# Kernel optimization log

Hardware: AMD Instinct MI355X
Metric: run time of the kernel (lower is better)

Reference implementation:

```python
import jax, jax.numpy as jnp
import numpy as np

N_HEADS = 16
THETA = 10000.0


def _rope(x, cos, sin):
    # x: [B,H,S,hd]; pairs are interleaved (x[...,2i], x[...,2i+1]) = complex pair
    xe = x[..., 0::2]
    xo = x[..., 1::2]
    re = xe * cos - xo * sin
    im = xe * sin + xo * cos
    return jnp.stack([re, im], axis=-1).reshape(x.shape)


def setup_inputs() -> dict:
    key = jax.random.key(0)
    k1, k2, k3 = jax.random.split(key, 3)
    B, S, D = 2, 2048, 2048
    x = jax.random.normal(k1, (B, S, D), dtype=jnp.float32)
    Wqkv = jax.random.normal(k2, (D, 3 * D), dtype=jnp.float32) * (D ** -0.5)
    Wo = jax.random.normal(k3, (D, D), dtype=jnp.float32) * (D ** -0.5)
    return {"x": x, "Wqkv": Wqkv, "Wo": Wo}


def reference(x, Wqkv, Wo):
    B, S, D = x.shape
    H = N_HEADS
    hd = D // H
    half = hd // 2

    qkv = x @ Wqkv                                   # [B,S,3D]
    q, k, v = jnp.split(qkv, 3, axis=-1)
    # [B,S,D] -> [B,H,S,hd]
    q = q.reshape(B, S, H, hd).transpose(0, 2, 1, 3)
    k = k.reshape(B, S, H, hd).transpose(0, 2, 1, 3)
    v = v.reshape(B, S, H, hd).transpose(0, 2, 1, 3)

    # RoPE frequencies: thetas = theta^(-2i/hd), freqs = pos outer thetas
    i = jnp.arange(half, dtype=jnp.float32)
    inv = THETA ** (-2.0 * i / hd)
    pos = jnp.arange(S, dtype=jnp.float32)
    freqs = pos[:, None] * inv[None, :]              # [S, half]
    cos = jnp.cos(freqs)[None, None]                 # [1,1,S,half]
    sin = jnp.sin(freqs)[None, None]
    q = _rope(q, cos, sin)
    k = _rope(k, cos, sin)

    scale = 1.0 / jnp.sqrt(jnp.float32(hd))
    scores = jnp.einsum("bhqd,bhkd->bhqk", q, k) * scale
    causal = jnp.tril(jnp.ones((S, S), dtype=bool))
    scores = jnp.where(causal[None, None], scores, -jnp.inf)
    attn = jax.nn.softmax(scores, axis=-1)
    y = jnp.einsum("bhqk,bhkd->bhqd", attn, v)       # [B,H,S,hd]
    y = y.transpose(0, 2, 1, 3).reshape(B, S, D)
    return y @ Wo
```

## Files before the change

kernel.cpp:

```cpp
#include <hip/hip_runtime.h>
#include <hip/hip_bf16.h>

typedef __attribute__((ext_vector_type(4))) float f32x4;
typedef __attribute__((ext_vector_type(8))) short s16x8;
typedef unsigned short u16;
typedef unsigned int u32;

#define MFMA16 __builtin_amdgcn_mfma_f32_16x16x32_bf16

#define GLL16(g, l)                                                        \
  __builtin_amdgcn_global_load_lds(                                        \
      (const __attribute__((address_space(1))) void*)(g),                  \
      (__attribute__((address_space(3))) void*)(l), 16, 0, 0)

__device__ __forceinline__ u16 f2b(float f) {
  u32 x = __builtin_bit_cast(u32, f);
  u32 r = (x + 0x7fffu + ((x >> 16) & 1u)) >> 16;
  return (u16)r;
}
__device__ __forceinline__ float b2f(u16 u) {
  u32 x = ((u32)u) << 16;
  return __builtin_bit_cast(float, x);
}

__global__ __launch_bounds__(256) void k_cvt(const float* __restrict__ in, u16* __restrict__ out) {
  size_t i = ((size_t)blockIdx.x * 256 + threadIdx.x) * 4;
  float4 v = *(const float4*)(in + i);
  ushort4 o; o.x = f2b(v.x); o.y = f2b(v.y); o.z = f2b(v.z); o.w = f2b(v.w);
  *(ushort4*)(out + i) = o;
}

__global__ __launch_bounds__(256) void k_tconv(const float* __restrict__ in, u16* __restrict__ out,
                                               int R, int C) {
  __shared__ u16 tile[64][72];
  int c0 = blockIdx.x * 64, r0 = blockIdx.y * 64;
  int t = threadIdx.x;
#pragma unroll
  for (int p = 0; p < 4; ++p) {
    int idx = p * 1024 + t * 4;
    int row = idx >> 6, col = idx & 63;
    float4 v = *(const float4*)&in[(size_t)(r0 + row) * C + c0 + col];
    tile[row][col]     = f2b(v.x);
    tile[row][col + 1] = f2b(v.y);
    tile[row][col + 2] = f2b(v.z);
    tile[row][col + 3] = f2b(v.w);
  }
  __syncthreads();
#pragma unroll
  for (int p = 0; p < 4; ++p) {
    int idx = p * 1024 + t * 4;
    int row = idx >> 6, col = idx & 63;
    ushort4 o;
    o.x = tile[col][row]; o.y = tile[col + 1][row];
    o.z = tile[col + 2][row]; o.w = tile[col + 3][row];
    *(ushort4*)&out[(size_t)(c0 + row) * R + r0 + col] = o;
  }
}

__global__ __launch_bounds__(256) void k_trv(const u16* __restrict__ v, u16* __restrict__ vt) {
  __shared__ u16 tile[64][72];
  int bh = blockIdx.z;
  int s0 = blockIdx.x * 64, d0 = blockIdx.y * 64;
  const u16* src = v + (size_t)bh * 2048 * 128;
  u16* dst = vt + (size_t)bh * 2048 * 128;
  int t = threadIdx.x;
#pragma unroll
  for (int p = 0; p < 4; ++p) {
    int idx = p * 1024 + t * 4;
    int row = idx >> 6, col = idx & 63;
    ushort4 x = *(const ushort4*)&src[(size_t)(s0 + row) * 128 + d0 + col];
    tile[row][col] = x.x; tile[row][col + 1] = x.y;
    tile[row][col + 2] = x.z; tile[row][col + 3] = x.w;
  }
  __syncthreads();
#pragma unroll
  for (int p = 0; p < 4; ++p) {
    int idx = p * 1024 + t * 4;
    int row = idx >> 6, col = idx & 63;
    ushort4 o;
    o.x = tile[col][row]; o.y = tile[col + 1][row];
    o.z = tile[col + 2][row]; o.w = tile[col + 3][row];
    *(ushort4*)&dst[(size_t)(d0 + row) * 2048 + s0 + col] = o;
  }
}

__global__ __launch_bounds__(256) void k_trig(float2* __restrict__ tab) {
  int t = blockIdx.x * 256 + threadIdx.x;
  int s = t >> 6, i = t & 63;
  float inv = expf(-(float)i * (9.210340371976184f / 64.f));
  float a = (float)s * inv;
  float sn, cs;
  sincosf(a, &sn, &cs);
  tab[t] = make_float2(cs, sn);
}

__global__ __launch_bounds__(256) void k_rope(u16* __restrict__ q, u16* __restrict__ k,
                                              const float2* __restrict__ tab) {
  u16* ptr = blockIdx.y ? k : q;
  size_t tid = (size_t)blockIdx.x * 256 + threadIdx.x;
  int g = (int)(tid & 15);
  int s = (int)((tid >> 4) & 2047);
  int bh = (int)(tid >> 15);
  size_t base = ((size_t)bh * 2048 + s) * 128 + (size_t)g * 8;
  uint4 dv = *(const uint4*)(ptr + base);
  u16* pu = (u16*)&dv;
  const float2* tb = &tab[s * 64 + g * 4];
#pragma unroll
  for (int j = 0; j < 4; ++j) {
    float xe = b2f(pu[2 * j]), xo = b2f(pu[2 * j + 1]);
    float c = tb[j].x, sn = tb[j].y;
    pu[2 * j]     = f2b(xe * c - xo * sn);
    pu[2 * j + 1] = f2b(xe * sn + xo * c);
  }
  *(uint4*)(ptr + base) = dv;
}

template <int MODE>
__global__ __launch_bounds__(512) void k_gemm8(const u16* __restrict__ A, const u16* __restrict__ Bt,
                                               u16* __restrict__ qo, u16* __restrict__ ko,
                                               u16* __restrict__ vo, float* __restrict__ C) {
  constexpr int K = 2048;
  constexpr int NT = K / 64;
  __shared__ u16 sA[3][128 * 64];
  __shared__ u16 sB[3][256 * 64];
  int tid = threadIdx.x;
  int lane = tid & 63, w = tid >> 6;
  int wr = w >> 2, wc = w & 3;
  int lr = lane & 15, lg = lane >> 4;

  int n0 = blockIdx.x * 256;
  int m0 = blockIdx.y * 128;

  int srow = tid >> 3;
  int swzcolb = ((tid & 7) << 4) ^ ((srow & 7) << 4);
  const char* gA = (const char*)(A + (size_t)(m0 + srow) * K) + swzcolb;
  const char* gB = (const char*)(Bt + (size_t)(n0 + srow) * K) + swzcolb;

#define STAGE8(buf, k0)                                                      \
  {                                                                          \
    _Pragma("unroll") for (int rb = 0; rb < 4; ++rb)                         \
        GLL16(gB + ((size_t)rb * 64 * K + (k0)) * 2,                         \
              (char*)&sB[buf][0] + rb * 8192 + tid * 16);                    \
    _Pragma("unroll") for (int ra = 0; ra < 2; ++ra)                         \
        GLL16(gA + ((size_t)ra * 64 * K + (k0)) * 2,                         \
              (char*)&sA[buf][0] + ra * 8192 + tid * 16);                    \
  }

  int colb0 = (lg << 4) ^ ((lr & 7) << 4);
  int aRowByte = (wr * 64 + lr) * 128;
  int bRowByte = (wc * 64 + lr) * 128;

  f32x4 acc[4][4] = {};

  STAGE8(0, 0);
  STAGE8(1, 64);

  for (int t = 0; t < NT; ++t) {
    int cur = t % 3;
    const char* sAb = (const char*)&sA[0][0] + cur * (128 * 64 * 2);
    const char* sBb = (const char*)&sB[0][0] + cur * (256 * 64 * 2);
    if (t + 1 < NT) { asm volatile("s_waitcnt vmcnt(6)" ::: "memory"); }
    else            { asm volatile("s_waitcnt vmcnt(0)" ::: "memory"); }
    __builtin_amdgcn_s_barrier();
    if (t + 2 < NT) STAGE8((t + 2) % 3, (t + 2) * 64);
    s16x8 af[4], bf[4];
#pragma unroll
    for (int i = 0; i < 4; ++i) af[i] = *(const s16x8*)(sAb + aRowByte + i * 2048 + colb0);
#pragma unroll
    for (int i = 0; i < 4; ++i) bf[i] = *(const s16x8*)(sBb + bRowByte + i * 2048 + colb0);
    __builtin_amdgcn_s_barrier();
    asm volatile("s_waitcnt lgkmcnt(0)" ::: "memory");
    __builtin_amdgcn_sched_barrier(0);
    __builtin_amdgcn_s_setprio(1);
#pragma unroll
    for (int mi = 0; mi < 4; ++mi)
#pragma unroll
      for (int ni = 0; ni < 4; ++ni)
        acc[mi][ni] = MFMA16(af[mi], bf[ni], acc[mi][ni], 0, 0, 0);
    __builtin_amdgcn_s_setprio(0);
    __builtin_amdgcn_s_barrier();
#pragma unroll
    for (int i = 0; i < 4; ++i) af[i] = *(const s16x8*)(sAb + aRowByte + i * 2048 + (colb0 ^ 64));
#pragma unroll
    for (int i = 0; i < 4; ++i) bf[i] = *(const s16x8*)(sBb + bRowByte + i * 2048 + (colb0 ^ 64));
    __builtin_amdgcn_s_barrier();
    asm volatile("s_waitcnt lgkmcnt(0)" ::: "memory");
    __builtin_amdgcn_sched_barrier(0);
    __builtin_amdgcn_s_setprio(1);
#pragma unroll
    for (int mi = 0; mi < 4; ++mi)
#pragma unroll
      for (int ni = 0; ni < 4; ++ni)
        acc[mi][ni] = MFMA16(af[mi], bf[ni], acc[mi][ni], 0, 0, 0);
    __builtin_amdgcn_s_setprio(0);
  }
#undef STAGE8

  if constexpr (MODE == 0) {
#pragma unroll
    for (int ni = 0; ni < 4; ++ni) {
      int n = n0 + wc * 64 + ni * 16 + lr;
      int which = n >> 11;
      int h = (n >> 7) & 15;
      int d = n & 127;
      u16* dst = which == 0 ? qo : (which == 1 ? ko : vo);
#pragma unroll
      for (int mi = 0; mi < 4; ++mi)
#pragma unroll
        for (int r = 0; r < 4; ++r) {
          int m = m0 + wr * 64 + mi * 16 + lg * 4 + r;
          int b = m >> 11, s = m & 2047;
          dst[(((size_t)b * 16 + h) * 2048 + s) * 128 + d] = f2b(acc[mi][ni][r]);
        }
    }
  } else {
#pragma unroll
    for (int mi = 0; mi < 4; ++mi)
#pragma unroll
      for (int ni = 0; ni < 4; ++ni)
#pragma unroll
        for (int r = 0; r < 4; ++r) {
          int m = m0 + wr * 64 + mi * 16 + lg * 4 + r;
          int n = n0 + wc * 64 + ni * 16 + lr;
          C[(size_t)m * 2048 + n] = acc[mi][ni][r];
        }
  }
}

__global__ __launch_bounds__(256) void k_attn(const u16* __restrict__ q, const u16* __restrict__ k,
                                              const u16* __restrict__ vt, u16* __restrict__ y) {
  constexpr int S = 2048, HD = 128;
  __shared__ u16 kt[2][64][128];
  __shared__ u16 vtl[2][128][64];
  __shared__ u16 pl[4][16][72];
  int bh = blockIdx.x;
  int qt = (gridDim.y - 1) - blockIdx.y;
  int q0 = qt * 64;
  int t = threadIdx.x, lane = t & 63, w = t >> 6;
  int lr = lane & 15, lg = lane >> 4;
  const size_t base = (size_t)bh * S * HD;
  const u16* kbh = k + base;
  const u16* vbh = vt + base;

  int kr_l = ((w * 4) << 2) + (lane >> 4);
  int kcb_base = (lane & 15) << 4;
  int vr_l = ((w * 4) << 3) + (lane >> 3);
  int vcb_base = (lane & 7) << 4;

  s16x8 aq[4];
  {
    size_t qrow = base + (size_t)(q0 + w * 16 + lr) * HD;
#pragma unroll
    for (int i = 0; i < 4; ++i) aq[i] = *(const s16x8*)&q[qrow + i * 32 + lg * 8];
  }
  f32x4 o[8] = {};
  float mrow[4] = {-INFINITY, -INFINITY, -INFINITY, -INFINITY};
  float lsum[4] = {};
  const float scale = 0.08838834764831845f;
  int kv_end = q0 + 64;

#define STAGE_KV(buf, kv)                                                             \
  {                                                                                   \
    _Pragma("unroll")                                                                 \
    for (int i = 0; i < 4; ++i) {                                                     \
      int kr = kr_l + 4 * i;                                                          \
      int kcb = kcb_base ^ ((kr & 7) << 4);                                           \
      GLL16((const char*)(kbh + (size_t)((kv) + kr) * HD) + kcb,                      \
            (char*)&kt[buf][0][0] + ((w * 4 + i) << 10) + (lane << 4));               \
      int vr = vr_l + 8 * i;                                                          \
      int vcb = vcb_base ^ ((vr & 7) << 4);                                           \
      GLL16((const char*)(vbh + (size_t)vr * S + (kv)) + vcb,                         \
            (char*)&vtl[buf][0][0] + ((w * 4 + i) << 10) + (lane << 4));              \
    }                                                                                 \
  }

  STAGE_KV(0, 0);
  int cur = 0;
  for (int kv0 = 0; kv0 < kv_end; kv0 += 64) {
    __syncthreads();
    if (kv0 + 64 < kv_end) STAGE_KV(cur ^ 1, kv0 + 64);
    f32x4 sf[4] = {};
    int swz = (lr & 7) << 4;
    __builtin_amdgcn_s_setprio(1);
#pragma unroll
    for (int dstep = 0; dstep < 4; ++dstep)
#pragma unroll
      for (int nt = 0; nt < 4; ++nt) {
        int cb = ((dstep << 6) + (lg << 4)) ^ swz;
        s16x8 bk = *(const s16x8*)((const char*)&kt[cur][nt * 16 + lr][0] + cb);
        sf[nt] = MFMA16(aq[dstep], bk, sf[nt], 0, 0, 0);
      }
    __builtin_amdgcn_s_setprio(0);
    int grow0 = q0 + w * 16 + lg * 4;
    float pmax[4] = {-INFINITY, -INFINITY, -INFINITY, -INFINITY};
#pragma unroll
    for (int nt = 0; nt < 4; ++nt) {
      int col = kv0 + nt * 16 + lr;
#pragma unroll
      for (int r = 0; r < 4; ++r) {
        float sv = sf[nt][r] * scale;
        if (col > grow0 + r) sv = -INFINITY;
        sf[nt][r] = sv;
        pmax[r] = fmaxf(pmax[r], sv);
      }
    }
#pragma unroll
    for (int off = 1; off < 16; off <<= 1)
#pragma unroll
      for (int r = 0; r < 4; ++r) pmax[r] = fmaxf(pmax[r], __shfl_xor(pmax[r], off));
    float alpha[4], ps[4];
#pragma unroll
    for (int r = 0; r < 4; ++r) {
      float mn = fmaxf(mrow[r], pmax[r]);
      alpha[r] = __expf(mrow[r] - mn);
      mrow[r] = mn;
      ps[r] = 0.f;
#pragma unroll
      for (int nt = 0; nt < 4; ++nt) { float e = __expf(sf[nt][r] - mn); sf[nt][r] = e; ps[r] += e; }
    }
#pragma unroll
    for (int off = 1; off < 16; off <<= 1)
#pragma unroll
      for (int r = 0; r < 4; ++r) ps[r] += __shfl_xor(ps[r], off);
#pragma unroll
    for (int r = 0; r < 4; ++r) {
      lsum[r] = lsum[r] * alpha[r] + ps[r];
#pragma unroll
      for (int dt = 0; dt < 8; ++dt) o[dt][r] *= alpha[r];
    }
#pragma unroll
    for (int nt = 0; nt < 4; ++nt)
#pragma unroll
      for (int r = 0; r < 4; ++r)
        pl[w][lg * 4 + r][nt * 16 + lr] = f2b(sf[nt][r]);
    asm volatile("s_waitcnt lgkmcnt(0)" ::: "memory");
    __builtin_amdgcn_sched_barrier(0);
    s16x8 pa0 = *(const s16x8*)&pl[w][lr][lg * 8];
    s16x8 pa1 = *(const s16x8*)&pl[w][lr][32 + lg * 8];
    __builtin_amdgcn_s_setprio(1);
#pragma unroll
    for (int dt = 0; dt < 8; ++dt) {
      int cb0 = (lg << 4) ^ swz;
      int cb1 = (64 + (lg << 4)) ^ swz;
      s16x8 bv0 = *(const s16x8*)((const char*)&vtl[cur][dt * 16 + lr][0] + cb0);
      s16x8 bv1 = *(const s16x8*)((const char*)&vtl[cur][dt * 16 + lr][0] + cb1);
      o[dt] = MFMA16(pa0, bv0, o[dt], 0, 0, 0);
      o[dt] = MFMA16(pa1, bv1, o[dt], 0, 0, 0);
    }
    __builtin_amdgcn_s_setprio(0);
    cur ^= 1;
  }
#undef STAGE_KV
  int b = bh >> 4, h = bh & 15;
#pragma unroll
  for (int dt = 0; dt < 8; ++dt)
#pragma unroll
    for (int r = 0; r < 4; ++r) {
      int srow = q0 + w * 16 + lg * 4 + r;
      float val = o[dt][r] / lsum[r];
      y[((size_t)(b * 2048 + srow)) * 2048 + h * 128 + dt * 16 + lr] = f2b(val);
    }
}

extern "C" void kernel_launch(void* const* d_in, const int* in_sizes, int n_in,
                              void* d_out, int out_size, void* d_ws, size_t ws_size,
                              hipStream_t stream) {
  const float* x    = (const float*)d_in[0];
  const float* wqkv = (const float*)d_in[1];
  const float* wo   = (const float*)d_in[2];
  float* out = (float*)d_out;
  char* ws = (char*)d_ws;
  u16* xb    = (u16*)(ws);
  u16* wqkvt = (u16*)(ws + (size_t)(16)  * 1048576);
  u16* wot   = (u16*)(ws + (size_t)(40)  * 1048576);
  u16* qb    = (u16*)(ws + (size_t)(48)  * 1048576);
  u16* kb    = (u16*)(ws + (size_t)(64)  * 1048576);
  u16* vb    = (u16*)(ws + (size_t)(80)  * 1048576);
  u16* vtb   = (u16*)(ws + (size_t)(96)  * 1048576);
  u16* yb    = (u16*)(ws + (size_t)(112) * 1048576);
  float2* trig = (float2*)(ws + (size_t)(128) * 1048576);

  k_cvt<<<8192, 256, 0, stream>>>(x, xb);
  k_tconv<<<dim3(96, 32), 256, 0, stream>>>(wqkv, wqkvt, 2048, 6144);
  k_tconv<<<dim3(32, 32), 256, 0, stream>>>(wo, wot, 2048, 2048);
  k_trig<<<512, 256, 0, stream>>>(trig);
  k_gemm8<0><<<dim3(24, 32), 512, 0, stream>>>(xb, wqkvt, qb, kb, vb, nullptr);
  k_rope<<<dim3(4096, 2), 256, 0, stream>>>(qb, kb, trig);
  k_trv<<<dim3(32, 2, 32), 256, 0, stream>>>(vb, vtb);
  k_attn<<<dim3(32, 32), 256, 0, stream>>>(qb, kb, vtb, yb);
  k_gemm8<1><<<dim3(8, 32), 512, 0, stream>>>(yb, wot, nullptr, nullptr, nullptr, out);
}
```

Baseline: 334.0 us.

## Replace triple-buffered 128x256 GEMM with single-buffered 128x128 tile kernel

Replaces the 512-thread, triple-buffered 128x256 GEMM with a simpler 256-thread 128x128 kernel that loads one K-tile into LDS and syncs between loads and compute, so global loads no longer overlap with MFMA work. Smaller tiles and LDS use mean twice as many blocks and likely more resident blocks per CU, which the change relies on to hide load latency. The QKV epilogue now derives the q/k/v target and head from blockIdx. The risk is exposed load latency with no software pipelining and more redundant global traffic from the smaller N tile.

```diff
diff --git a/kernel.cpp b/kernel.cpp
--- a/kernel.cpp
+++ b/kernel.cpp
@@ -116,103 +116,68 @@
 }
 
 template <int MODE>
-__global__ __launch_bounds__(512) void k_gemm8(const u16* __restrict__ A, const u16* __restrict__ Bt,
-                                               u16* __restrict__ qo, u16* __restrict__ ko,
-                                               u16* __restrict__ vo, float* __restrict__ C) {
+__global__ __launch_bounds__(256) void k_gemm97b(const u16* __restrict__ A, const u16* __restrict__ Bt,
+                                                 u16* __restrict__ qo, u16* __restrict__ ko,
+                                                 u16* __restrict__ vo, float* __restrict__ C) {
   constexpr int K = 2048;
-  constexpr int NT = K / 64;
-  __shared__ u16 sA[3][128 * 64];
-  __shared__ u16 sB[3][256 * 64];
+  __shared__ u16 sa[128 * 64];
+  __shared__ u16 sb[128 * 64];
   int tid = threadIdx.x;
   int lane = tid & 63, w = tid >> 6;
-  int wr = w >> 2, wc = w & 3;
+  int wm = (w >> 1) * 64, wn = (w & 1) * 64;
   int lr = lane & 15, lg = lane >> 4;
-
-  int n0 = blockIdx.x * 256;
+  int n0 = blockIdx.x * 128;
   int m0 = blockIdx.y * 128;
 
   int srow = tid >> 3;
-  int swzcolb = ((tid & 7) << 4) ^ ((srow & 7) << 4);
-  const char* gA = (const char*)(A + (size_t)(m0 + srow) * K) + swzcolb;
-  const char* gB = (const char*)(Bt + (size_t)(n0 + srow) * K) + swzcolb;
-
-#define STAGE8(buf, k0)                                                      \
-  {                                                                          \
-    _Pragma("unroll") for (int rb = 0; rb < 4; ++rb)                         \
-        GLL16(gB + ((size_t)rb * 64 * K + (k0)) * 2,                         \
-              (char*)&sB[buf][0] + rb * 8192 + tid * 16);                    \
-    _Pragma("unroll") for (int ra = 0; ra < 2; ++ra)                         \
-        GLL16(gA + ((size_t)ra * 64 * K + (k0)) * 2,                         \
-              (char*)&sA[buf][0] + ra * 8192 + tid * 16);                    \
-  }
+  int swzb = ((tid & 7) << 4) ^ ((srow & 7) << 4);
+  const char* gA = (const char*)(A + (size_t)(m0 + srow) * K) + swzb;
+  const char* gB = (const char*)(Bt + (size_t)(n0 + srow) * K) + swzb;
 
   int colb0 = (lg << 4) ^ ((lr & 7) << 4);
-  int aRowByte = (wr * 64 + lr) * 128;
-  int bRowByte = (wc * 64 + lr) * 128;
+  int aRowB = (wm + lr) * 128;
+  int bRowB = (wn + lr) * 128;
 
   f32x4 acc[4][4] = {};
-
-  STAGE8(0, 0);
-  STAGE8(1, 64);
-
-  for (int t = 0; t < NT; ++t) {
-    int cur = t % 3;
-    const char* sAb = (const char*)&sA[0][0] + cur * (128 * 64 * 2);
-    const char* sBb = (const char*)&sB[0][0] + cur * (256 * 64 * 2);
-    if (t + 1 < NT) { asm volatile("s_waitcnt vmcnt(6)" ::: "memory"); }
-    else            { asm volatile("s_waitcnt vmcnt(0)" ::: "memory"); }
-    __builtin_amdgcn_s_barrier();
-    if (t + 2 < NT) STAGE8((t + 2) % 3, (t + 2) * 64);
-    s16x8 af[4], bf[4];
-#pragma unroll
-    for (int i = 0; i < 4; ++i) af[i] = *(const s16x8*)(sAb + aRowByte + i * 2048 + colb0);
-#pragma unroll
-    for (int i = 0; i < 4; ++i) bf[i] = *(const s16x8*)(sBb + bRowByte + i * 2048 + colb0);
-    __builtin_amdgcn_s_barrier();
-    asm volatile("s_waitcnt lgkmcnt(0)" ::: "memory");
-    __builtin_amdgcn_sched_barrier(0);
-    __builtin_amdgcn_s_setprio(1);
+  for (int k0 = 0; k0 < K; k0 += 64) {
+    __syncthreads();
+#pragma unroll
+    for (int r = 0; r < 4; ++r) {
+      GLL16(gA + ((size_t)(r * 32) * K + k0) * 2, (char*)sa + r * 4096 + tid * 16);
+      GLL16(gB + ((size_t)(r * 32) * K + k0) * 2, (char*)sb + r * 4096 + tid * 16);
+    }
+    __syncthreads();
+#pragma unroll
+    for (int ks = 0; ks < 2; ++ks) {
+      int cb = colb0 ^ (ks << 6);
+      s16x8 af[4], bf[4];
+#pragma unroll
+      for (int i = 0; i < 4; ++i) af[i] = *(const s16x8*)((const char*)sa + aRowB + i * 2048 + cb);
+#pragma unroll
+      for (int i = 0; i < 4; ++i) bf[i] = *(const s16x8*)((const char*)sb + bRowB + i * 2048 + cb);
+#pragma unroll
+      for (int mi = 0; mi < 4; ++mi)
+#pragma unroll
+        for (int ni = 0; ni < 4; ++ni)
+          acc[mi][ni] = MFMA16(af[mi], bf[ni], acc[mi][ni], 0, 0, 0);
+    }
+  }
+
+  if constexpr (MODE == 0) {
+    int which = blockIdx.x >> 4;
+    int h = blockIdx.x & 15;
+    u16* dst = which == 0 ? qo : (which == 1 ? ko : vo);
 #pragma unroll
     for (int mi = 0; mi < 4; ++mi)
 #pragma unroll
       for (int ni = 0; ni < 4; ++ni)
-        acc[mi][ni] = MFMA16(af[mi], bf[ni], acc[mi][ni], 0, 0, 0);
-    __builtin_amdgcn_s_setprio(0);
-    __builtin_amdgcn_s_barrier();
-#pragma unroll
-    for (int i = 0; i < 4; ++i) af[i] = *(const s16x8*)(sAb + aRowByte + i * 2048 + (colb0 ^ 64));
-#pragma unroll
-    for (int i = 0; i < 4; ++i) bf[i] = *(const s16x8*)(sBb + bRowByte + i * 2048 + (colb0 ^ 64));
-    __builtin_amdgcn_s_barrier();
-    asm volatile("s_waitcnt lgkmcnt(0)" ::: "memory");
-    __builtin_amdgcn_sched_barrier(0);
-    __builtin_amdgcn_s_setprio(1);
-#pragma unroll
-    for (int mi = 0; mi < 4; ++mi)
-#pragma unroll
-      for (int ni = 0; ni < 4; ++ni)
-        acc[mi][ni] = MFMA16(af[mi], bf[ni], acc[mi][ni], 0, 0, 0);
-    __builtin_amdgcn_s_setprio(0);
-  }
-#undef STAGE8
-
-  if constexpr (MODE == 0) {
-#pragma unroll
-    for (int ni = 0; ni < 4; ++ni) {
-      int n = n0 + wc * 64 + ni * 16 + lr;
-      int which = n >> 11;
-      int h = (n >> 7) & 15;
-      int d = n & 127;
-      u16* dst = which == 0 ? qo : (which == 1 ? ko : vo);
-#pragma unroll
-      for (int mi = 0; mi < 4; ++mi)
 #pragma unroll
         for (int r = 0; r < 4; ++r) {
-          int m = m0 + wr * 64 + mi * 16 + lg * 4 + r;
+          int m = m0 + wm + mi * 16 + lg * 4 + r;
+          int d = wn + ni * 16 + lr;
           int b = m >> 11, s = m & 2047;
           dst[(((size_t)b * 16 + h) * 2048 + s) * 128 + d] = f2b(acc[mi][ni][r]);
         }
-    }
   } else {
 #pragma unroll
     for (int mi = 0; mi < 4; ++mi)
@@ -220,8 +185,8 @@
       for (int ni = 0; ni < 4; ++ni)
 #pragma unroll
         for (int r = 0; r < 4; ++r) {
-          int m = m0 + wr * 64 + mi * 16 + lg * 4 + r;
-          int n = n0 + wc * 64 + ni * 16 + lr;
+          int m = m0 + wm + mi * 16 + lg * 4 + r;
+          int n = n0 + wn + ni * 16 + lr;
           C[(size_t)m * 2048 + n] = acc[mi][ni][r];
         }
   }
@@ -384,9 +349,9 @@
   k_tconv<<<dim3(96, 32), 256, 0, stream>>>(wqkv, wqkvt, 2048, 6144);
   k_tconv<<<dim3(32, 32), 256, 0, stream>>>(wo, wot, 2048, 2048);
   k_trig<<<512, 256, 0, stream>>>(trig);
-  k_gemm8<0><<<dim3(24, 32), 512, 0, stream>>>(xb, wqkvt, qb, kb, vb, nullptr);
+  k_gemm97b<0><<<dim3(48, 32), 256, 0, stream>>>(xb, wqkvt, qb, kb, vb, nullptr);
   k_rope<<<dim3(4096, 2), 256, 0, stream>>>(qb, kb, trig);
   k_trv<<<dim3(32, 2, 32), 256, 0, stream>>>(vb, vtb);
   k_attn<<<dim3(32, 32), 256, 0, stream>>>(qb, kb, vtb, yb);
-  k_gemm8<1><<<dim3(8, 32), 512, 0, stream>>>(yb, wot, nullptr, nullptr, nullptr, out);
-}
+  k_gemm97b<1><<<dim3(16, 32), 256, 0, stream>>>(yb, wot, nullptr, nullptr, nullptr, out);
+}
```

Measured after the change: 285.5 us. 1.17x faster.
